# Performance work log

Hardware: AMD Instinct MI355X
Metric: run time of the kernel (lower is better)

## Reference

```python
import jax, jax.numpy as jnp
import numpy as np

B, S, D, H = 2, 4096, 512, 8
HD = D // H


def setup_inputs() -> dict:
    key = jax.random.key(0)
    ks = jax.random.split(key, 11)
    s = 1.0 / np.sqrt(D)
    return {
        "queries": jax.random.normal(ks[0], (B, S, D), jnp.float32),
        "keys": jax.random.normal(ks[1], (B, S, D), jnp.float32),
        "values": jax.random.normal(ks[2], (B, S, D), jnp.float32),
        "Wq": jax.random.normal(ks[3], (D, D), jnp.float32) * s,
        "bq": jnp.zeros((D,), jnp.float32),
        "Wk": jax.random.normal(ks[4], (D, D), jnp.float32) * s,
        "bk": jnp.zeros((D,), jnp.float32),
        "Wv": jax.random.normal(ks[5], (D, D), jnp.float32) * s,
        "bv": jnp.zeros((D,), jnp.float32),
        "Wo": jax.random.normal(ks[6], (D, D), jnp.float32) * s,
        "bo": jnp.zeros((D,), jnp.float32),
    }


def reference(queries, keys, values, Wq, bq, Wk, bk, Wv, bv, Wo, bo):
    b = queries.shape[0]
    # Linear projections (torch Linear: x @ W.T + b; here W stored as [in, out])
    q = (queries @ Wq + bq).reshape(b, -1, H, HD)   # [B, Sq, H, HD]
    k = (keys @ Wk + bk).reshape(b, -1, H, HD)       # [B, Sk, H, HD]
    v = (values @ Wv + bv).reshape(b, -1, H, HD)     # [B, Sk, H, HD]
    logits = jnp.einsum('bqhd,bkhd->bhqk', q, k) / jnp.sqrt(jnp.float32(HD))
    attn = jax.nn.softmax(logits, axis=-1)           # [B, H, Sq, Sk]  (dropout_rate=0 -> identity)
    ctx = jnp.einsum('bhqk,bkhd->bqhd', attn, v).reshape(b, -1, H * HD)
    return ctx @ Wo + bo
```

## Files before the change

### kernel.cpp

```cpp
#include <hip/hip_runtime.h>
#include <hip/hip_bf16.h>

constexpr int B_  = 2;
constexpr int S_  = 4096;
constexpr int D_  = 512;
constexpr int H_  = 8;
constexpr int HD_ = 64;
constexpr int M_  = B_ * S_;

typedef __attribute__((ext_vector_type(8))) short short8;
typedef __attribute__((ext_vector_type(4))) float floatx4;

static __device__ __forceinline__ unsigned short f2bf(float f) {
    union { float f; unsigned u; } v; v.f = f;
    unsigned r = v.u + 0x7fffu + ((v.u >> 16) & 1u);
    return (unsigned short)(r >> 16);
}

static __device__ __forceinline__ unsigned pk2bf(float a, float b) {
#if __has_builtin(__builtin_amdgcn_cvt_pk_bf16_f32)
    typedef __attribute__((ext_vector_type(2))) __bf16 bf16x2_t;
    union { bf16x2_t v; unsigned u; } u;
    u.v = __builtin_amdgcn_cvt_pk_bf16_f32(a, b);
    return u.u;
#else
    return (unsigned)f2bf(a) | ((unsigned)f2bf(b) << 16);
#endif
}

#if __has_builtin(__builtin_amdgcn_exp2f)
#define EXP2(x) __builtin_amdgcn_exp2f(x)
#else
#define EXP2(x) exp2f(x)
#endif

#define QSCALE 0.18033688011110204f

static __device__ __forceinline__ void gl_lds16(const void* g, void* l) {
    typedef __attribute__((address_space(1))) const unsigned GU;
    typedef __attribute__((address_space(3))) unsigned LU;
    __builtin_amdgcn_global_load_lds((GU*)g, (LU*)l, 16, 0, 0);
}

__global__ __launch_bounds__(256) void prep_kernel(
    const float* __restrict__ Xq, const float* __restrict__ Xk, const float* __restrict__ Xv,
    const float* __restrict__ Wq, const float* __restrict__ Wk,
    const float* __restrict__ Wv, const float* __restrict__ Wo,
    unsigned short* __restrict__ Y,
    unsigned short* __restrict__ T) {
    const int bid = blockIdx.x;
    const int t   = threadIdx.x;
    __shared__ float Tt[64][65];

    if (bid < 1536) {
        const int z   = bid / 512;
        const int blk = bid - z * 512;
        const float* X = z == 0 ? Xq : (z == 1 ? Xk : Xv);
        unsigned short* Yz = Y + (size_t)z * M_ * D_;
        const int n8 = M_ * D_ / 8;
        for (int i = blk * 256 + t; i < n8; i += 512 * 256) {
            float4 a = *(const float4*)&X[(size_t)i * 8];
            float4 b = *(const float4*)&X[(size_t)i * 8 + 4];
            union { short8 s; unsigned u[4]; } p;
            p.u[0] = pk2bf(a.x, a.y); p.u[1] = pk2bf(a.z, a.w);
            p.u[2] = pk2bf(b.x, b.y); p.u[3] = pk2bf(b.z, b.w);
            *(short8*)&Yz[(size_t)i * 8] = p.s;
        }
    } else {
        const int b2 = bid - 1536;
        const int z  = b2 >> 6;
        const int rm = b2 & 63;
        const int k0 = (rm >> 3) * 64, n0 = (rm & 7) * 64;
        const float* W = z == 0 ? Wq : (z == 1 ? Wk : (z == 2 ? Wv : Wo));
        unsigned short* Wt = T + (size_t)z * D_ * D_;
#pragma unroll
        for (int i = 0; i < 4; ++i) {
            const int flat = t + 256 * i;
            const int kr = flat >> 4, nc = (flat & 15) * 4;
            float4 v = *(const float4*)&W[(size_t)(k0 + kr) * 512 + n0 + nc];
            Tt[kr][nc] = v.x; Tt[kr][nc + 1] = v.y;
            Tt[kr][nc + 2] = v.z; Tt[kr][nc + 3] = v.w;
        }
        __syncthreads();
#pragma unroll
        for (int i = 0; i < 4; ++i) {
            const int flat = t + 256 * i;
            const int nr = flat >> 4, kc = (flat & 15) * 4;
            ushort4 o4;
            o4.x = f2bf(Tt[kc][nr]);     o4.y = f2bf(Tt[kc + 1][nr]);
            o4.z = f2bf(Tt[kc + 2][nr]); o4.w = f2bf(Tt[kc + 3][nr]);
            *(ushort4*)&Wt[(size_t)(n0 + nr) * 512 + k0 + kc] = o4;
        }
    }
}

template <int MODE>
__global__ __launch_bounds__(256, 3) void gemm_kernel(
    const unsigned short* __restrict__ Ab,
    const unsigned short* __restrict__ Wt,
    const float* __restrict__ b0, const float* __restrict__ b1, const float* __restrict__ b2,
    unsigned short* __restrict__ o0, unsigned short* __restrict__ o1,
    unsigned short* __restrict__ o2, float* __restrict__ of) {
    __shared__ unsigned short As[128 * 64];
    __shared__ unsigned short Bs[128 * 64];

    const int tid  = threadIdx.x;
    const int w    = tid >> 6;
    const int lane = tid & 63;
    const int n0   = blockIdx.x * 128;
    const int m0   = blockIdx.y * 128;
    const int lm   = lane & 15;
    const int lq   = lane >> 4;
    const int lm7  = lm & 7;
    const int wm   = (w >> 1) * 64;
    const int wn   = (w & 1) * 64;

    const int z = MODE == 0 ? (n0 >> 9) : 0;
    const unsigned short* A = MODE == 0 ? Ab + (size_t)z * M_ * D_ : Ab;

    const int srow = lane >> 3;
    const int slc  = ((lane & 7) ^ (srow & 7)) * 8;

    floatx4 acc[4][4];
#pragma unroll
    for (int i = 0; i < 4; ++i)
#pragma unroll
        for (int j = 0; j < 4; ++j) acc[i][j] = (floatx4)0.0f;

    for (int kb = 0; kb < 8; ++kb) {
        const int k0 = kb * 64;
        __syncthreads();
#pragma unroll
        for (int it = 0; it < 4; ++it) {
            const int r8 = w * 32 + it * 8;
            gl_lds16(&A [(size_t)(m0 + r8 + srow) * 512 + k0 + slc], &As[r8 * 64]);
            gl_lds16(&Wt[(size_t)(n0 + r8 + srow) * 512 + k0 + slc], &Bs[r8 * 64]);
        }
        __syncthreads();

        short8 af[2][4], bf[2][4];
#pragma unroll
        for (int ks = 0; ks < 2; ++ks)
#pragma unroll
            for (int i = 0; i < 4; ++i) {
                const int cc = ((ks * 4 + lq) ^ lm7) * 8;
                af[ks][i] = *(const short8*)&As[(wm + i * 16 + lm) * 64 + cc];
                bf[ks][i] = *(const short8*)&Bs[(wn + i * 16 + lm) * 64 + cc];
            }
#pragma unroll
        for (int ks = 0; ks < 2; ++ks)
#pragma unroll
            for (int mi = 0; mi < 4; ++mi)
#pragma unroll
                for (int ni = 0; ni < 4; ++ni)
                    acc[mi][ni] = __builtin_amdgcn_mfma_f32_16x16x32_bf16(
                        af[ks][mi], bf[ks][ni], acc[mi][ni], 0, 0, 0);
    }

    const float* bias = MODE == 0 ? (z == 0 ? b0 : (z == 1 ? b1 : b2)) : b0;
    const float scale = (MODE == 0 && z == 0) ? QSCALE : 1.0f;
    const int nl0 = n0 & 511;

    float bias_n[4];
#pragma unroll
    for (int ni = 0; ni < 4; ++ni) bias_n[ni] = bias[nl0 + wn + ni * 16 + lm];

#pragma unroll
    for (int mi = 0; mi < 4; ++mi) {
#pragma unroll
        for (int ni = 0; ni < 4; ++ni) {
            if (MODE == 1) {
                const int gn = n0 + wn + ni * 16 + lm;
#pragma unroll
                for (int r = 0; r < 4; ++r) {
                    const int gm = m0 + wm + mi * 16 + lq * 4 + r;
                    of[(size_t)gm * 512 + gn] = acc[mi][ni][r] + bias_n[ni];
                }
            } else {
                const int gnl = nl0 + wn + ni * 16 + lm;
                if (z == 2) {
                    const int h = gnl >> 6, hd = gnl & 63;
                    const int gm = m0 + wm + mi * 16 + lq * 4;
                    const int b = gm >> 12, s = gm & 4095;
                    union { ushort4 s4; uint2 u; } o4;
                    o4.u.x = pk2bf(acc[mi][ni][0] + bias_n[ni], acc[mi][ni][1] + bias_n[ni]);
                    o4.u.y = pk2bf(acc[mi][ni][2] + bias_n[ni], acc[mi][ni][3] + bias_n[ni]);
                    *(ushort4*)&o2[(((size_t)(b * 8 + h)) * 64 + hd) * 4096 + s] = o4.s4;
                } else {
                    unsigned short* out = z == 0 ? o0 : o1;
#pragma unroll
                    for (int r = 0; r < 4; ++r) {
                        const int gm = m0 + wm + mi * 16 + lq * 4 + r;
                        out[(size_t)gm * 512 + gnl] =
                            f2bf((acc[mi][ni][r] + bias_n[ni]) * scale);
                    }
                }
            }
        }
    }
}

__global__ __launch_bounds__(256) void flash_kernel(
    const unsigned short* __restrict__ Q, const unsigned short* __restrict__ K,
    const unsigned short* __restrict__ Vt, unsigned short* __restrict__ ctx) {
    __shared__ unsigned short Ks[2][64 * 64];
    __shared__ unsigned short Vs[2][64 * 64];
    __shared__ unsigned short Ps[4][16 * 64];

    const int tid = threadIdx.x;
    const int w   = tid >> 6;
    const int l   = tid & 63;
    const int lm  = l & 15;
    const int lq  = l >> 4;
    const int lm7 = lm & 7;
    const int q0  = blockIdx.x * 128;
    const int bh  = blockIdx.y;
    const int b   = bh >> 3, h = bh & 7;

    const unsigned short* Vg = Vt + (size_t)bh * HD_ * S_;
    const size_t rowbase = (size_t)b * 4096;

    short8 qf[2][2];
#pragma unroll
    for (int qn = 0; qn < 2; ++qn) {
        const unsigned short* qp =
            &Q[(rowbase + q0 + w * 32 + qn * 16 + lm) * 512 + h * 64];
        qf[qn][0] = *(const short8*)(qp + lq * 8);
        qf[qn][1] = *(const short8*)(qp + 32 + lq * 8);
    }

    short8 ones8;
#pragma unroll
    for (int j = 0; j < 8; ++j) ones8[j] = (short)0x3F80;

    floatx4 o[2][4];
#pragma unroll
    for (int qn = 0; qn < 2; ++qn)
#pragma unroll
        for (int i = 0; i < 4; ++i) o[qn][i] = (floatx4)0.0f;
    floatx4 ls[2];
    ls[0] = (floatx4)0.0f; ls[1] = (floatx4)0.0f;

    const int srow = l >> 3;
    const int slc  = ((l & 7) ^ (srow & 7)) * 8;

#define STAGE(T0, BUF)                                                         \
    {                                                                          \
        _Pragma("unroll") for (int it = 0; it < 2; ++it) {                     \
            const int r8 = w * 16 + it * 8;                                    \
            gl_lds16(&K[(rowbase + (T0) + r8 + srow) * 512 + h * 64 + slc],    \
                     &Ks[BUF][r8 * 64]);                                       \
            gl_lds16(&Vg[(size_t)(r8 + srow) * 4096 + (T0) + slc],            \
                     &Vs[BUF][r8 * 64]);                                       \
        }                                                                      \
    }

    STAGE(0, 0);
    __syncthreads();

    unsigned short* Pw = &Ps[w][0];

    for (int kt = 0; kt < 64; ++kt) {
        const int cur = kt & 1;
        if (kt < 63) STAGE((kt + 1) * 64, cur ^ 1);

        short8 kf[2][4];
#pragma unroll
        for (int ks = 0; ks < 2; ++ks)
#pragma unroll
            for (int ni = 0; ni < 4; ++ni)
                kf[ks][ni] = *(const short8*)&Ks[cur][(ni * 16 + lm) * 64 +
                                                      (((ks * 4 + lq) ^ lm7) * 8)];
        short8 vf[2][4];
#pragma unroll
        for (int c = 0; c < 2; ++c)
#pragma unroll
            for (int mt = 0; mt < 4; ++mt)
                vf[c][mt] = *(const short8*)&Vs[cur][(mt * 16 + lm) * 64 +
                                                     (((c * 4 + lq) ^ lm7) * 8)];

#pragma unroll
        for (int qn = 0; qn < 2; ++qn) {
            floatx4 sf[4];
#pragma unroll
            for (int ni = 0; ni < 4; ++ni) sf[ni] = (floatx4)0.0f;
#pragma unroll
            for (int ks = 0; ks < 2; ++ks)
#pragma unroll
                for (int ni = 0; ni < 4; ++ni)
                    sf[ni] = __builtin_amdgcn_mfma_f32_16x16x32_bf16(
                        kf[ks][ni], qf[qn][ks], sf[ni], 0, 0, 0);

#pragma unroll
            for (int ni = 0; ni < 4; ++ni) {
                uint2 pv;
                pv.x = pk2bf(EXP2(sf[ni][0]), EXP2(sf[ni][1]));
                pv.y = pk2bf(EXP2(sf[ni][2]), EXP2(sf[ni][3]));
                *(uint2*)&Pw[lm * 64 + (((ni * 2 + (lq >> 1)) ^ lm7) * 8) + (lq & 1) * 4] = pv;
            }
#pragma unroll
            for (int c = 0; c < 2; ++c) {
                short8 pf = *(const short8*)&Pw[lm * 64 + (((c * 4 + lq) ^ lm7) * 8)];
                ls[qn] = __builtin_amdgcn_mfma_f32_16x16x32_bf16(ones8, pf, ls[qn], 0, 0, 0);
#pragma unroll
                for (int mt = 0; mt < 4; ++mt)
                    o[qn][mt] = __builtin_amdgcn_mfma_f32_16x16x32_bf16(
                        vf[c][mt], pf, o[qn][mt], 0, 0, 0);
            }
        }
        __syncthreads();
    }

#pragma unroll
    for (int qn = 0; qn < 2; ++qn) {
        const float inv = 1.0f / ls[qn][0];
        const int q = q0 + w * 32 + qn * 16 + lm;
        const size_t rb = (rowbase + q) * 512 + h * 64;
#pragma unroll
        for (int mt = 0; mt < 4; ++mt) {
            union { ushort4 s; uint2 u; } o4;
            o4.u.x = pk2bf(o[qn][mt][0] * inv, o[qn][mt][1] * inv);
            o4.u.y = pk2bf(o[qn][mt][2] * inv, o[qn][mt][3] * inv);
            *(ushort4*)&ctx[rb + mt * 16 + lq * 4] = o4.s;
        }
    }
}

extern "C" void kernel_launch(void* const* d_in, const int* in_sizes, int n_in,
                              void* d_out, int out_size, void* d_ws, size_t ws_size,
                              hipStream_t stream) {
    const float* queries = (const float*)d_in[0];
    const float* keys    = (const float*)d_in[1];
    const float* values  = (const float*)d_in[2];
    const float* Wq = (const float*)d_in[3];
    const float* bq = (const float*)d_in[4];
    const float* Wk = (const float*)d_in[5];
    const float* bk = (const float*)d_in[6];
    const float* Wv = (const float*)d_in[7];
    const float* bv = (const float*)d_in[8];
    const float* Wo = (const float*)d_in[9];
    const float* bo = (const float*)d_in[10];

    unsigned short* xb    = (unsigned short*)d_ws;
    unsigned short* wsctx = xb;
    unsigned short* wsq   = xb   + (size_t)3 * M_ * D_;
    unsigned short* wsk   = wsq  + (size_t)M_ * D_;
    unsigned short* wsvt  = wsk  + (size_t)M_ * D_;
    unsigned short* wt    = wsvt + (size_t)M_ * D_;
    unsigned short* wto   = wt   + (size_t)3 * D_ * D_;

    prep_kernel<<<dim3(1792), dim3(256), 0, stream>>>(
        queries, keys, values, Wq, Wk, Wv, Wo, xb, wt);

    gemm_kernel<0><<<dim3(12, 64), dim3(256), 0, stream>>>(
        xb, wt, bq, bk, bv, wsq, wsk, wsvt, nullptr);

    flash_kernel<<<dim3(S_ / 128, B_ * H_), dim3(256), 0, stream>>>(
        wsq, wsk, wsvt, wsctx);

    gemm_kernel<1><<<dim3(4, 64), dim3(256), 0, stream>>>(
        wsctx, wto, bo, nullptr, nullptr, nullptr, nullptr, nullptr, (float*)d_out);
}
```

Before: 268.3 us.

## Store Q/K head-major and prefetch K/V tiles through registers in flash kernel

```diff
diff --git a/kernel.cpp b/kernel.cpp
--- a/kernel.cpp
+++ b/kernel.cpp
@@ -178,8 +178,8 @@
                 }
             } else {
                 const int gnl = nl0 + wn + ni * 16 + lm;
+                const int h = gnl >> 6, hd = gnl & 63;
                 if (z == 2) {
-                    const int h = gnl >> 6, hd = gnl & 63;
                     const int gm = m0 + wm + mi * 16 + lq * 4;
                     const int b = gm >> 12, s = gm & 4095;
                     union { ushort4 s4; uint2 u; } o4;
@@ -191,8 +191,9 @@
 #pragma unroll
                     for (int r = 0; r < 4; ++r) {
                         const int gm = m0 + wm + mi * 16 + lq * 4 + r;
-                        out[(size_t)gm * 512 + gnl] =
-                            f2bf((acc[mi][ni][r] + bias_n[ni]) * scale);
+                        const int b = gm >> 12, s = gm & 4095;
+                        const float vv = (acc[mi][ni][r] + bias_n[ni]) * scale;
+                        out[(((size_t)(b * 8 + h)) * 4096 + s) * 64 + hd] = f2bf(vv);
                     }
                 }
             }
@@ -205,7 +206,7 @@
     const unsigned short* __restrict__ Vt, unsigned short* __restrict__ ctx) {
     __shared__ unsigned short Ks[2][64 * 64];
     __shared__ unsigned short Vs[2][64 * 64];
-    __shared__ unsigned short Ps[4][16 * 64];
+    __shared__ unsigned short Ps[4][2][16 * 64];
 
     const int tid = threadIdx.x;
     const int w   = tid >> 6;
@@ -215,16 +216,16 @@
     const int lm7 = lm & 7;
     const int q0  = blockIdx.x * 128;
     const int bh  = blockIdx.y;
-    const int b   = bh >> 3, h = bh & 7;
-
-    const unsigned short* Vg = Vt + (size_t)bh * HD_ * S_;
-    const size_t rowbase = (size_t)b * 4096;
+
+    const size_t base = (size_t)bh * S_ * HD_;
+    const unsigned short* Qg = Q + base;
+    const unsigned short* Kg = K + base;
+    const unsigned short* Vg = Vt + base;
 
     short8 qf[2][2];
 #pragma unroll
     for (int qn = 0; qn < 2; ++qn) {
-        const unsigned short* qp =
-            &Q[(rowbase + q0 + w * 32 + qn * 16 + lm) * 512 + h * 64];
+        const unsigned short* qp = &Qg[(size_t)(q0 + w * 32 + qn * 16 + lm) * 64];
         qf[qn][0] = *(const short8*)(qp + lq * 8);
         qf[qn][1] = *(const short8*)(qp + 32 + lq * 8);
     }
@@ -241,28 +242,29 @@
     floatx4 ls[2];
     ls[0] = (floatx4)0.0f; ls[1] = (floatx4)0.0f;
 
-    const int srow = l >> 3;
-    const int slc  = ((l & 7) ^ (srow & 7)) * 8;
-
-#define STAGE(T0, BUF)                                                         \
-    {                                                                          \
-        _Pragma("unroll") for (int it = 0; it < 2; ++it) {                     \
-            const int r8 = w * 16 + it * 8;                                    \
-            gl_lds16(&K[(rowbase + (T0) + r8 + srow) * 512 + h * 64 + slc],    \
-                     &Ks[BUF][r8 * 64]);                                       \
-            gl_lds16(&Vg[(size_t)(r8 + srow) * 4096 + (T0) + slc],            \
-                     &Vs[BUF][r8 * 64]);                                       \
-        }                                                                      \
-    }
-
-    STAGE(0, 0);
+    const int sr   = tid >> 3, sch = tid & 7;
+    const int srcc = sch * 8;
+    const int swz  = ((sch ^ (sr & 7)) * 8);
+    const int sw0  = sr * 64 + swz;
+    const int sw1  = (sr + 32) * 64 + swz;
+
+    short8 kr0, kr1, vr0, vr1;
+    kr0 = *(const short8*)&Kg[(size_t)sr * 64 + srcc];
+    kr1 = *(const short8*)&Kg[(size_t)(sr + 32) * 64 + srcc];
+    vr0 = *(const short8*)&Vg[(size_t)sr * S_ + srcc];
+    vr1 = *(const short8*)&Vg[(size_t)(sr + 32) * S_ + srcc];
+    *(short8*)&Ks[0][sw0] = kr0;
+    *(short8*)&Ks[0][sw1] = kr1;
+    *(short8*)&Vs[0][sw0] = vr0;
+    *(short8*)&Vs[0][sw1] = vr1;
     __syncthreads();
-
-    unsigned short* Pw = &Ps[w][0];
+    kr0 = *(const short8*)&Kg[(size_t)(64 + sr) * 64 + srcc];
+    kr1 = *(const short8*)&Kg[(size_t)(64 + sr + 32) * 64 + srcc];
+    vr0 = *(const short8*)&Vg[(size_t)sr * S_ + 64 + srcc];
+    vr1 = *(const short8*)&Vg[(size_t)(sr + 32) * S_ + 64 + srcc];
 
     for (int kt = 0; kt < 64; ++kt) {
         const int cur = kt & 1;
-        if (kt < 63) STAGE((kt + 1) * 64, cur ^ 1);
 
         short8 kf[2][4];
 #pragma unroll
@@ -279,43 +281,65 @@
                 vf[c][mt] = *(const short8*)&Vs[cur][(mt * 16 + lm) * 64 +
                                                      (((c * 4 + lq) ^ lm7) * 8)];
 
-#pragma unroll
-        for (int qn = 0; qn < 2; ++qn) {
-            floatx4 sf[4];
-#pragma unroll
-            for (int ni = 0; ni < 4; ++ni) sf[ni] = (floatx4)0.0f;
-#pragma unroll
-            for (int ks = 0; ks < 2; ++ks)
+        floatx4 sf[2][4];
+#pragma unroll
+        for (int qn = 0; qn < 2; ++qn)
+#pragma unroll
+            for (int ni = 0; ni < 4; ++ni) sf[qn][ni] = (floatx4)0.0f;
+#pragma unroll
+        for (int ks = 0; ks < 2; ++ks)
+#pragma unroll
+            for (int qn = 0; qn < 2; ++qn)
 #pragma unroll
                 for (int ni = 0; ni < 4; ++ni)
-                    sf[ni] = __builtin_amdgcn_mfma_f32_16x16x32_bf16(
-                        kf[ks][ni], qf[qn][ks], sf[ni], 0, 0, 0);
-
+                    sf[qn][ni] = __builtin_amdgcn_mfma_f32_16x16x32_bf16(
+                        kf[ks][ni], qf[qn][ks], sf[qn][ni], 0, 0, 0);
+
+#pragma unroll
+        for (int qn = 0; qn < 2; ++qn)
 #pragma unroll
             for (int ni = 0; ni < 4; ++ni) {
                 uint2 pv;
-                pv.x = pk2bf(EXP2(sf[ni][0]), EXP2(sf[ni][1]));
-                pv.y = pk2bf(EXP2(sf[ni][2]), EXP2(sf[ni][3]));
-                *(uint2*)&Pw[lm * 64 + (((ni * 2 + (lq >> 1)) ^ lm7) * 8) + (lq & 1) * 4] = pv;
+                pv.x = pk2bf(EXP2(sf[qn][ni][0]), EXP2(sf[qn][ni][1]));
+                pv.y = pk2bf(EXP2(sf[qn][ni][2]), EXP2(sf[qn][ni][3]));
+                *(uint2*)&Ps[w][qn][lm * 64 + (((ni * 2 + (lq >> 1)) ^ lm7) * 8) +
+                                    (lq & 1) * 4] = pv;
             }
+
+#pragma unroll
+        for (int qn = 0; qn < 2; ++qn)
 #pragma unroll
             for (int c = 0; c < 2; ++c) {
-                short8 pf = *(const short8*)&Pw[lm * 64 + (((c * 4 + lq) ^ lm7) * 8)];
+                short8 pf = *(const short8*)&Ps[w][qn][lm * 64 + (((c * 4 + lq) ^ lm7) * 8)];
                 ls[qn] = __builtin_amdgcn_mfma_f32_16x16x32_bf16(ones8, pf, ls[qn], 0, 0, 0);
 #pragma unroll
                 for (int mt = 0; mt < 4; ++mt)
                     o[qn][mt] = __builtin_amdgcn_mfma_f32_16x16x32_bf16(
                         vf[c][mt], pf, o[qn][mt], 0, 0, 0);
             }
+
+        if (kt < 63) {
+            *(short8*)&Ks[cur ^ 1][sw0] = kr0;
+            *(short8*)&Ks[cur ^ 1][sw1] = kr1;
+            *(short8*)&Vs[cur ^ 1][sw0] = vr0;
+            *(short8*)&Vs[cur ^ 1][sw1] = vr1;
         }
         __syncthreads();
-    }
-
+        if (kt < 62) {
+            const int t2 = (kt + 2) * 64;
+            kr0 = *(const short8*)&Kg[(size_t)(t2 + sr) * 64 + srcc];
+            kr1 = *(const short8*)&Kg[(size_t)(t2 + sr + 32) * 64 + srcc];
+            vr0 = *(const short8*)&Vg[(size_t)sr * S_ + t2 + srcc];
+            vr1 = *(const short8*)&Vg[(size_t)(sr + 32) * S_ + t2 + srcc];
+        }
+    }
+
+    const int b = bh >> 3, h = bh & 7;
 #pragma unroll
     for (int qn = 0; qn < 2; ++qn) {
         const float inv = 1.0f / ls[qn][0];
         const int q = q0 + w * 32 + qn * 16 + lm;
-        const size_t rb = (rowbase + q) * 512 + h * 64;
+        const size_t rb = ((size_t)(b * S_ + q)) * 512 + h * 64;
 #pragma unroll
         for (int mt = 0; mt < 4; ++mt) {
             union { ushort4 s; uint2 u; } o4;
```

Result: faster. 249.2 us (-7.1%).
